# Kernel tuning notes

Hardware: AMD Instinct MI355X
Metric: run time of the kernel (lower is better)

## Reference

```python
import jax, jax.numpy as jnp
import numpy as np

B, N, R = 8, 1024, 8192
D_IN, REL_D = 32, 1
NF_P, NF_R, NF_E, D_OUT = 128, 128, 128, 3
PSTEP = 3


def setup_inputs() -> dict:
    key = jax.random.key(0)
    ks = jax.random.split(key, 26)
    state = jax.random.normal(ks[0], (B, N, D_IN), dtype=jnp.float32)
    # Rr/Rs are one-hot selection matrices [B, N, R]: column j selects the
    # receiver/sender particle of relation j.
    recv = jax.random.randint(ks[1], (B, R), 0, N)
    send = jax.random.randint(ks[2], (B, R), 0, N)
    Rr = jnp.transpose(jax.nn.one_hot(recv, N, dtype=jnp.float32), (0, 2, 1))
    Rs = jnp.transpose(jax.nn.one_hot(send, N, dtype=jnp.float32), (0, 2, 1))
    Ra = jax.random.normal(ks[3], (B, R, REL_D), dtype=jnp.float32)

    def lin(k, i, o):
        kw, kb = jax.random.split(k)
        return (0.02 * jax.random.normal(kw, (i, o), dtype=jnp.float32),
                0.02 * jax.random.normal(kb, (o,), dtype=jnp.float32))

    pe_w0, pe_b0 = lin(ks[4], D_IN, NF_P)
    pe_w1, pe_b1 = lin(ks[5], NF_P, NF_E)
    re_w0, re_b0 = lin(ks[6], 2 * D_IN + REL_D, NF_R)
    re_w1, re_b1 = lin(ks[7], NF_R, NF_R)
    re_w2, re_b2 = lin(ks[8], NF_R, NF_R)
    rp_w, rp_b = lin(ks[9], NF_R + 2 * NF_E, NF_E)   # relation_propagator
    pp_w, pp_b = lin(ks[10], 2 * NF_E, NF_E)          # particle_propagator
    pr_w0, pr_b0 = lin(ks[11], NF_E, NF_E)            # particle_predictor
    pr_w1, pr_b1 = lin(ks[12], NF_E, D_OUT)
    return dict(state=state, Rr=Rr, Rs=Rs, Ra=Ra, pstep=PSTEP,
                pe_w0=pe_w0, pe_b0=pe_b0, pe_w1=pe_w1, pe_b1=pe_b1,
                re_w0=re_w0, re_b0=re_b0, re_w1=re_w1, re_b1=re_b1,
                re_w2=re_w2, re_b2=re_b2, rp_w=rp_w, rp_b=rp_b,
                pp_w=pp_w, pp_b=pp_b, pr_w0=pr_w0, pr_b0=pr_b0,
                pr_w1=pr_w1, pr_b1=pr_b1)


def reference(state, Rr, Rs, Ra, pstep,
              pe_w0, pe_b0, pe_w1, pe_b1,
              re_w0, re_b0, re_w1, re_b1, re_w2, re_b2,
              rp_w, rp_b, pp_w, pp_b,
              pr_w0, pr_b0, pr_w1, pr_b1):
    relu = jax.nn.relu
    # gather particle states into relation slots: Rr^T @ state -> [B, R, D]
    state_r = jnp.einsum('bnr,bnd->brd', Rr, state)
    state_s = jnp.einsum('bnr,bnd->brd', Rs, state)
    # particle encoder: Linear-ReLU-Linear-ReLU
    particle_encode = relu(relu(state @ pe_w0 + pe_b0) @ pe_w1 + pe_b1)  # [B,N,NF_E]
    # relation encoder: 3-layer MLP with ReLU after each layer
    rel_in = jnp.concatenate([state_r, state_s, Ra], axis=2)
    h = relu(rel_in @ re_w0 + re_b0)
    h = relu(h @ re_w1 + re_b1)
    relation_encode = relu(h @ re_w2 + re_b2)  # [B,R,NF_R]

    particle_effect = jnp.zeros((B, N, NF_E), dtype=state.dtype)
    for _ in range(pstep):
        effect_r = jnp.einsum('bnr,bne->bre', Rr, particle_effect)  # gather
        effect_s = jnp.einsum('bnr,bne->bre', Rs, particle_effect)
        rel_x = jnp.concatenate([relation_encode, effect_r, effect_s], axis=2)
        relation_effect = relu(rel_x @ rp_w + rp_b)  # [B,R,NF_E]
        # scatter-add relation effects back to receiver particles
        effect_agg = jnp.einsum('bnr,bre->bne', Rr, relation_effect)
        part_x = jnp.concatenate([particle_encode, effect_agg], axis=2)
        # residual particle propagator: relu(linear(x) + prev_effect)
        particle_effect = relu(part_x @ pp_w + pp_b + particle_effect)
    pred = relu(particle_effect @ pr_w0 + pr_b0) @ pr_w1 + pr_b1  # [B,N,D_OUT]
    return pred
```

## Files before the change

kernel.cpp:

```cpp
#include <hip/hip_runtime.h>

#define NB 8
#define NP 1024
#define NR 8192

typedef unsigned short u16;
typedef __attribute__((ext_vector_type(8))) short bf16x8;
typedef __attribute__((ext_vector_type(4))) float f32x4;
typedef __attribute__((ext_vector_type(4))) unsigned int u32x4;

#define MFMA __builtin_amdgcn_mfma_f32_16x16x32_bf16

static __device__ __forceinline__ float bf2f(u16 u) {
    union { unsigned int i; float f; } v; v.i = ((unsigned int)u) << 16; return v.f;
}
static __device__ __forceinline__ unsigned int f2bf(float f) {
    union { float fv; unsigned int i; } v; v.fv = f;
    unsigned int r = v.i + 0x7FFFu + ((v.i >> 16) & 1u);
    return r >> 16;
}
static __device__ __forceinline__ unsigned int pack2(float a, float b) {
    return f2bf(a) | (f2bf(b) << 16);
}
static __device__ __forceinline__ void unpk8(uint4 v, float* o) {
    o[0] = bf2f((u16)(v.x & 0xFFFF)); o[1] = bf2f((u16)(v.x >> 16));
    o[2] = bf2f((u16)(v.y & 0xFFFF)); o[3] = bf2f((u16)(v.y >> 16));
    o[4] = bf2f((u16)(v.z & 0xFFFF)); o[5] = bf2f((u16)(v.z >> 16));
    o[6] = bf2f((u16)(v.w & 0xFFFF)); o[7] = bf2f((u16)(v.w >> 16));
}

template<int KC>
static __device__ __forceinline__ void load_wfrag(
    const bf16x8* __restrict__ fb, bf16x8 (&wf)[KC][2], int tid)
{
    #pragma unroll
    for (int kc = 0; kc < KC; ++kc)
      #pragma unroll
      for (int nt = 0; nt < 2; ++nt)
        wf[kc][nt] = fb[(kc*2 + nt)*256 + tid];
}

template<int MT, int KC, int LDA>
static __device__ __forceinline__ void mfma_compute(
    const u16* xlds, const bf16x8 (&wf)[KC][2], f32x4 (&acc)[MT][2],
    int l16, int quad)
{
    #pragma unroll
    for (int kc = 0; kc < KC; ++kc) {
        bf16x8 a[MT];
        #pragma unroll
        for (int mt = 0; mt < MT; ++mt)
            a[mt] = *(const bf16x8*)(xlds + (mt*16 + l16)*LDA + kc*32 + quad*8);
        #pragma unroll
        for (int mt = 0; mt < MT; ++mt) {
            acc[mt][0] = MFMA(a[mt], wf[kc][0], acc[mt][0], 0, 0, 0);
            acc[mt][1] = MFMA(a[mt], wf[kc][1], acc[mt][1], 0, 0, 0);
        }
    }
}

template<int MT>
static __device__ __forceinline__ void zero_acc(f32x4 (&acc)[MT][2]) {
    #pragma unroll
    for (int mt = 0; mt < MT; ++mt)
      #pragma unroll
      for (int nt = 0; nt < 2; ++nt)
        acc[mt][nt] = f32x4{0.f, 0.f, 0.f, 0.f};
}

template<int MT, int LDA>
static __device__ __forceinline__ void store_c_lds(
    u16* xlds, const f32x4 (&acc)[MT][2], const float* __restrict__ bias,
    int wave, int quad, int l16, int coloff = 0)
{
    #pragma unroll
    for (int mt = 0; mt < MT; ++mt)
      #pragma unroll
      for (int nt = 0; nt < 2; ++nt) {
        int col = wave*32 + nt*16 + l16;
        float bv = bias[col];
        #pragma unroll
        for (int rg = 0; rg < 4; ++rg)
            xlds[(mt*16 + quad*4 + rg)*LDA + coloff + col] =
                (u16)f2bf(fmaxf(acc[mt][nt][rg] + bv, 0.f));
      }
}

template<int MT, bool RELU>
static __device__ __forceinline__ void store_c_glob(
    u16* __restrict__ out, long row0, const f32x4 (&acc)[MT][2],
    const float* __restrict__ bias, int wave, int quad, int l16)
{
    #pragma unroll
    for (int mt = 0; mt < MT; ++mt)
      #pragma unroll
      for (int nt = 0; nt < 2; ++nt) {
        int col = wave*32 + nt*16 + l16;
        float bv = bias[col];
        #pragma unroll
        for (int rg = 0; rg < 4; ++rg) {
            long r = row0 + mt*16 + quad*4 + rg;
            float v = acc[mt][nt][rg] + bv;
            if (RELU) v = fmaxf(v, 0.f);
            out[r*128 + col] = (u16)f2bf(v);
        }
      }
}

__global__ __launch_bounds__(256) void k_idxprep(
    const u32x4* __restrict__ Rr4, const u32x4* __restrict__ Rs4,
    u16* __restrict__ recv, u16* __restrict__ send,
    const float* __restrict__ w0, const float* __restrict__ w1,
    const float* __restrict__ w2, const float* __restrict__ w3,
    const float* __restrict__ w4, const float* __restrict__ w5,
    const float* __restrict__ w6, const float* __restrict__ w7,
    bf16x8* __restrict__ wfrag,
    const float* __restrict__ state, const float* __restrict__ pe_b0,
    const float* __restrict__ pe_b1, u16* __restrict__ penc)
{
    constexpr int LDA = 136;
    __shared__ __align__(16) u16 xlds[64 * LDA];
    int tid = threadIdx.x;
    const int wave = tid >> 6, quad = (tid >> 4) & 3, l16 = tid & 15;

    if (blockIdx.x < 8) {
        const float* W; int KC, kv, off;
        switch (blockIdx.x) {
            case 0:  W = w0; KC = 3;  kv = 65;  off = 0;  break;
            case 1:  W = w1; KC = 4;  kv = 128; off = 6;  break;
            case 2:  W = w2; KC = 4;  kv = 128; off = 14; break;
            case 3:  W = w3; KC = 1;  kv = 32;  off = 22; break;
            case 4:  W = w4; KC = 4;  kv = 128; off = 24; break;
            case 5:  W = w5; KC = 12; kv = 384; off = 32; break;
            case 6:  W = w6; KC = 8;  kv = 256; off = 56; break;
            default: W = w7; KC = 4;  kv = 128; off = 72; break;
        }
        for (int kc = 0; kc < KC; ++kc)
          for (int nt = 0; nt < 2; ++nt) {
            bf16x8 f;
            #pragma unroll
            for (int j = 0; j < 8; ++j) {
                int k = kc*32 + quad*8 + j;
                f[j] = (k < kv) ? (short)f2bf(W[k*128 + wave*32 + nt*16 + l16]) : (short)0;
            }
            wfrag[(off + kc*2 + nt)*256 + tid] = f;
          }
        return;
    }

    if (blockIdx.x < 136) {
        const long row0 = (long)(blockIdx.x - 8) * 64;
        for (int idx = tid; idx < 64 * 8; idx += 256) {
            int r = idx >> 3, c = idx & 7;
            float4 v = *(const float4*)(state + (row0 + r)*32 + c*4);
            uint2 o; o.x = pack2(v.x, v.y); o.y = pack2(v.z, v.w);
            *(uint2*)(xlds + r*LDA + c*4) = o;
        }
        __syncthreads();
        f32x4 acc[4][2];
        zero_acc<4>(acc);
        {
            bf16x8 wf[1][2];
            #pragma unroll
            for (int nt = 0; nt < 2; ++nt)
              #pragma unroll
              for (int j = 0; j < 8; ++j) {
                int k = quad*8 + j;
                wf[0][nt][j] = (short)f2bf(w3[k*128 + wave*32 + nt*16 + l16]);
              }
            mfma_compute<4, 1, LDA>(xlds, wf, acc, l16, quad);
        }
        __syncthreads();
        store_c_lds<4, LDA>(xlds, acc, pe_b0, wave, quad, l16);
        __syncthreads();
        zero_acc<4>(acc);
        {
            bf16x8 wf[4][2];
            #pragma unroll
            for (int kc = 0; kc < 4; ++kc)
              #pragma unroll
              for (int nt = 0; nt < 2; ++nt)
                #pragma unroll
                for (int j = 0; j < 8; ++j) {
                    int k = kc*32 + quad*8 + j;
                    wf[kc][nt][j] = (short)f2bf(w4[k*128 + wave*32 + nt*16 + l16]);
                }
            mfma_compute<4, 4, LDA>(xlds, wf, acc, l16, quad);
        }
        store_c_glob<4, true>(penc, row0, acc, pe_b1, wave, quad, l16);
        return;
    }

    int sid = blockIdx.x - 136;
    int mat = sid & 1;
    const u32x4* src = mat ? Rs4 : Rr4;
    u16* dst = mat ? send : recv;
    long base = (long)(sid >> 1) * 2048 + tid;
    u32x4 v[8];
    #pragma unroll
    for (int k = 0; k < 8; ++k)
        v[k] = __builtin_nontemporal_load(src + base + k*256);
    #pragma unroll
    for (int k = 0; k < 8; ++k) {
        long i = base + k*256;
        int c4 = (int)(i & 2047), n = (int)((i >> 11) & 1023), b = (int)(i >> 21);
        int o = b * NR + c4 * 4;
        if (v[k][0]) dst[o + 0] = (u16)n;
        if (v[k][1]) dst[o + 1] = (u16)n;
        if (v[k][2]) dst[o + 2] = (u16)n;
        if (v[k][3]) dst[o + 3] = (u16)n;
    }
}

__global__ __launch_bounds__(256) void k_csrenc(
    const float* __restrict__ state, const float* __restrict__ Ra,
    const u16* __restrict__ recv, const u16* __restrict__ send,
    int* __restrict__ row_ptr, unsigned int* __restrict__ pidx,
    const bf16x8* __restrict__ f_re0, const float* __restrict__ re_b0,
    const bf16x8* __restrict__ f_re1, const float* __restrict__ re_b1,
    const bf16x8* __restrict__ f_re2, const float* __restrict__ re_b2,
    const bf16x8* __restrict__ f_rpP, const float* __restrict__ rp_b,
    u16* __restrict__ bufP)
{
    constexpr int LDA = 136;
    __shared__ __align__(16) u16 xlds[64 * LDA];
    __shared__ int cur[NP];
    __shared__ int wsum[4];
    const int tid = threadIdx.x;

    if (blockIdx.x < 8) {
        const int b = blockIdx.x;
        for (int i = tid; i < NP; i += 256) cur[i] = 0;
        __syncthreads();
        int pv[32];
        #pragma unroll
        for (int k = 0; k < 32; ++k) {
            pv[k] = recv[b * NR + k * 256 + tid] & 1023;
            atomicAdd(&cur[pv[k]], 1);
        }
        __syncthreads();
        int4 c4v = ((const int4*)cur)[tid];
        int s = c4v.x + c4v.y + c4v.z + c4v.w;
        int si = s;
        #pragma unroll
        for (int off = 1; off < 64; off <<= 1) {
            int u = __shfl_up(si, off);
            if ((tid & 63) >= off) si += u;
        }
        if ((tid & 63) == 63) wsum[tid >> 6] = si;
        __syncthreads();
        if (tid == 0) {
            int a0 = 0;
            #pragma unroll
            for (int i = 0; i < 4; ++i) { int w = wsum[i]; wsum[i] = a0; a0 += w; }
        }
        __syncthreads();
        int base = si - s + wsum[tid >> 6];
        int e0 = base, e1 = base + c4v.x, e2 = e1 + c4v.y, e3 = e2 + c4v.z;
        int* rp = row_ptr + b * (NP + 1);
        rp[tid*4 + 0] = e0; rp[tid*4 + 1] = e1;
        rp[tid*4 + 2] = e2; rp[tid*4 + 3] = e3;
        cur[tid*4 + 0] = e0; cur[tid*4 + 1] = e1;
        cur[tid*4 + 2] = e2; cur[tid*4 + 3] = e3;
        if (tid == 255) rp[NP] = e3 + c4v.w;
        __syncthreads();
        #pragma unroll
        for (int k = 0; k < 32; ++k) {
            int r = k * 256 + tid;
            int j = atomicAdd(&cur[pv[k]], 1) & 8191;
            pidx[b * NR + j] = (unsigned int)(r & 8191)
                             | ((unsigned int)(send[b * NR + r] & 1023) << 16);
        }
        return;
    }

    const int wave = tid >> 6, quad = (tid >> 4) & 3, l16 = tid & 15;
    f32x4 acc[4][2];
    const int row0 = (blockIdx.x - 8) * 64;
    const int b = row0 >> 13;
    {
        int r = tid >> 2, tt = tid & 3;
        int rel = row0 + r;
        u16* dst = xlds + r * LDA;
        int ri = recv[rel] & 1023;
        int si = send[rel] & 1023;
        const float* rrow = state + ((long)(b*NP + ri)) * 32;
        const float* srow = state + ((long)(b*NP + si)) * 32;
        float4 a0 = *(const float4*)(rrow + tt*8);
        float4 a1 = *(const float4*)(rrow + tt*8 + 4);
        uint4 o;
        o.x = pack2(a0.x, a0.y); o.y = pack2(a0.z, a0.w);
        o.z = pack2(a1.x, a1.y); o.w = pack2(a1.z, a1.w);
        *(uint4*)(dst + tt*8) = o;
        float4 s0 = *(const float4*)(srow + tt*8);
        float4 s1 = *(const float4*)(srow + tt*8 + 4);
        o.x = pack2(s0.x, s0.y); o.y = pack2(s0.z, s0.w);
        o.z = pack2(s1.x, s1.y); o.w = pack2(s1.z, s1.w);
        *(uint4*)(dst + 32 + tt*8) = o;
        if (tt == 3) {
            uint4 z = make_uint4(0, 0, 0, 0);
            *(uint4*)(dst + 64) = z; *(uint4*)(dst + 72) = z;
            *(uint4*)(dst + 80) = z; *(uint4*)(dst + 88) = z;
            dst[64] = (u16)f2bf(Ra[rel]);
        }
    }
    __syncthreads();
    zero_acc<4>(acc);
    {
        bf16x8 wf[3][2];
        load_wfrag<3>(f_re0, wf, tid);
        mfma_compute<4, 3, LDA>(xlds, wf, acc, l16, quad);
    }
    __syncthreads();
    store_c_lds<4, LDA>(xlds, acc, re_b0, wave, quad, l16);
    __syncthreads();
    zero_acc<4>(acc);
    {
        bf16x8 wf[4][2];
        load_wfrag<4>(f_re1, wf, tid);
        mfma_compute<4, 4, LDA>(xlds, wf, acc, l16, quad);
    }
    __syncthreads();
    store_c_lds<4, LDA>(xlds, acc, re_b1, wave, quad, l16);
    __syncthreads();
    zero_acc<4>(acc);
    {
        bf16x8 wf[4][2];
        load_wfrag<4>(f_re2, wf, tid);
        mfma_compute<4, 4, LDA>(xlds, wf, acc, l16, quad);
    }
    __syncthreads();
    store_c_lds<4, LDA>(xlds, acc, re_b2, wave, quad, l16);
    __syncthreads();
    zero_acc<4>(acc);
    {
        bf16x8 wf[4][2];
        load_wfrag<4>(f_rpP, wf, tid);
        mfma_compute<4, 4, LDA>(xlds, wf, acc, l16, quad);
    }
    #pragma unroll
    for (int mt = 0; mt < 4; ++mt)
      #pragma unroll
      for (int nt = 0; nt < 2; ++nt) {
        int col = wave*32 + nt*16 + l16;
        float bv = rp_b[col];
        #pragma unroll
        for (int rg = 0; rg < 4; ++rg) {
            int rl = mt*16 + quad*4 + rg;
            bufP[((long)(row0 + rl))*128 + col] = (u16)f2bf(acc[mt][nt][rg] + bv);
        }
      }
}

template<bool STEP1, bool MAKEUV, bool LAST>
__global__ __launch_bounds__(256) void k_pp(
    const u16* __restrict__ penc, const u16* __restrict__ bufP,
    const u16* __restrict__ UV_in, u16* __restrict__ UV_out,
    const int* __restrict__ row_ptr, const unsigned int* __restrict__ pidx,
    const bf16x8* __restrict__ f_pp, const float* __restrict__ pp_b,
    const bf16x8* __restrict__ f_U, const bf16x8* __restrict__ f_V,
    const bf16x8* __restrict__ f_pr0, const float* __restrict__ pr_b0,
    const float* __restrict__ pr_w1, const float* __restrict__ pr_b1,
    float* __restrict__ peff32_io, float* __restrict__ out)
{
    constexpr int LDA = 264;
    __shared__ __align__(16) u16 xlds[16 * LDA];
    const int tid = threadIdx.x;
    const int wave = tid >> 6, quad = (tid >> 4) & 3, l16 = tid & 15;
    const long row0 = (long)blockIdx.x * 16;

    {
        int r = tid >> 4, c = tid & 15;
        *(uint4*)(xlds + r*LDA + c*8) = *(const uint4*)(penc + (row0 + r)*128 + c*8);
    }
    {
        int pp = tid >> 4;
        int cq = tid & 15;
        int gp = (int)row0 + pp;
        int b = gp >> 10, pl = gp & 1023;
        const int* rp = row_ptr + b * (NP + 1);
        int s0 = rp[pl], e0 = rp[pl + 1];
        const unsigned int* pidxb = pidx + b * NR;
        const u16* bufPb = bufP + (long)b * NR * 128;
        float a[8];
        #pragma unroll
        for (int t = 0; t < 8; ++t) a[t] = 0.f;
        float uv[8];
        if (!STEP1) {
            const u16* ur = UV_in + ((long)gp)*256 + cq*8;
            unpk8(*(const uint4*)ur, uv);
        }
        const u16* uvb = UV_in + ((long)(b*NP))*256 + 128 + cq*8;
        for (int jb = s0; jb < e0; jb += 4) {
            int m = e0 - jb; if (m > 4) m = 4;
            unsigned int ids[4];
            #pragma unroll
            for (int t = 0; t < 4; ++t) {
                int j = jb + t; if (j > e0 - 1) j = e0 - 1;
                ids[t] = pidxb[j];
            }
            uint4 P0[4], V0[4];
            #pragma unroll
            for (int t = 0; t < 4; ++t) {
                P0[t] = *(const uint4*)(bufPb + ((long)(ids[t] & 8191u))*128 + cq*8);
                if (!STEP1)
                    V0[t] = *(const uint4*)(uvb + (long)((ids[t] >> 16) & 1023u)*256);
            }
            #pragma unroll
            for (int t = 0; t < 4; ++t) {
                if (t < m) {
                    float pv[8];
                    unpk8(P0[t], pv);
                    if (STEP1) {
                        #pragma unroll
                        for (int e = 0; e < 8; ++e) a[e] += fmaxf(pv[e], 0.f);
                    } else {
                        float vv[8];
                        unpk8(V0[t], vv);
                        #pragma unroll
                        for (int e = 0; e < 8; ++e)
                            a[e] += fmaxf(pv[e] + uv[e] + vv[e], 0.f);
                    }
                }
            }
        }
        u16* dst = xlds + pp*LDA + 128 + cq*8;
        uint4 o;
        o.x = pack2(a[0], a[1]); o.y = pack2(a[2], a[3]);
        o.z = pack2(a[4], a[5]); o.w = pack2(a[6], a[7]);
        *(uint4*)dst = o;
    }
    __syncthreads();

    f32x4 acc[1][2];
    {
        bf16x8 wf[8][2];
        load_wfrag<8>(f_pp, wf, tid);
        zero_acc<1>(acc);
        mfma_compute<1, 8, LDA>(xlds, wf, acc, l16, quad);
    }
    __syncthreads();

    #pragma unroll
    for (int nt = 0; nt < 2; ++nt) {
        int col = wave*32 + nt*16 + l16;
        float bv = pp_b[col];
        #pragma unroll
        for (int rg = 0; rg < 4; ++rg) {
            int rloc = quad*4 + rg;
            long r = row0 + rloc;
            float prev = STEP1 ? 0.f : peff32_io[r*128 + col];
            float v = fmaxf(acc[0][nt][rg] + bv + prev, 0.f);
            if (!LAST) peff32_io[r*128 + col] = v;
            xlds[rloc*LDA + col] = (u16)f2bf(v);
        }
    }
    __syncthreads();

    if (MAKEUV) {
        #pragma unroll
        for (int half = 0; half < 2; ++half) {
            bf16x8 wf[4][2];
            load_wfrag<4>(half ? f_V : f_U, wf, tid);
            zero_acc<1>(acc);
            mfma_compute<1, 4, LDA>(xlds, wf, acc, l16, quad);
            #pragma unroll
            for (int nt = 0; nt < 2; ++nt) {
                int col = half*128 + wave*32 + nt*16 + l16;
                #pragma unroll
                for (int rg = 0; rg < 4; ++rg) {
                    long r = row0 + quad*4 + rg;
                    UV_out[r*256 + col] = (u16)f2bf(acc[0][nt][rg]);
                }
            }
        }
    }
    if (LAST) {
        bf16x8 wf[4][2];
        load_wfrag<4>(f_pr0, wf, tid);
        zero_acc<1>(acc);
        mfma_compute<1, 4, LDA>(xlds, wf, acc, l16, quad);
        store_c_lds<1, LDA>(xlds, acc, pr_b0, wave, quad, l16, 128);
        __syncthreads();
        if (tid < 48) {
            int row = tid / 3, col = tid - row * 3;
            float s = pr_b1[col];
            const u16* hr = xlds + row * LDA + 128;
            #pragma unroll 8
            for (int k = 0; k < 128; ++k) s += bf2f(hr[k]) * pr_w1[k*3 + col];
            out[(row0 + row)*3 + col] = s;
        }
    }
}

extern "C" void kernel_launch(void* const* d_in, const int* in_sizes, int n_in,
                              void* d_out, int out_size, void* d_ws, size_t ws_size,
                              hipStream_t stream) {
    const float* state = (const float*)d_in[0];
    const float* Rr    = (const float*)d_in[1];
    const float* Rs    = (const float*)d_in[2];
    const float* Ra    = (const float*)d_in[3];
    const float* pe_w0 = (const float*)d_in[5];
    const float* pe_b0 = (const float*)d_in[6];
    const float* pe_w1 = (const float*)d_in[7];
    const float* pe_b1 = (const float*)d_in[8];
    const float* re_w0 = (const float*)d_in[9];
    const float* re_b0 = (const float*)d_in[10];
    const float* re_w1 = (const float*)d_in[11];
    const float* re_b1 = (const float*)d_in[12];
    const float* re_w2 = (const float*)d_in[13];
    const float* re_b2 = (const float*)d_in[14];
    const float* rp_w  = (const float*)d_in[15];
    const float* rp_b  = (const float*)d_in[16];
    const float* pp_w  = (const float*)d_in[17];
    const float* pp_b  = (const float*)d_in[18];
    const float* pr_w0 = (const float*)d_in[19];
    const float* pr_b0 = (const float*)d_in[20];
    const float* pr_w1 = (const float*)d_in[21];
    const float* pr_b1 = (const float*)d_in[22];

    char* p = (char*)d_ws;
    u16*    bufP    = (u16*)p;    p += (size_t)NB*NR*128*2;
    u16*    UVa     = (u16*)p;    p += (size_t)NB*NP*256*2;
    u16*    UVb     = (u16*)p;    p += (size_t)NB*NP*256*2;
    float*  peff32  = (float*)p;  p += (size_t)NB*NP*128*4;
    u16*    penc    = (u16*)p;    p += (size_t)NB*NP*128*2;
    bf16x8* wfrag   = (bf16x8*)p; p += (size_t)80*256*16;
    int*    row_ptr = (int*)p;    p += (size_t)NB*(NP+1)*4 + 12;
    u16*    recv    = (u16*)p;    p += (size_t)NB*NR*2;
    u16*    send    = (u16*)p;    p += (size_t)NB*NR*2;
    unsigned int* pidx = (unsigned int*)p; p += (size_t)NB*NR*4;

    const bf16x8* f_re0 = wfrag + 0*256;
    const bf16x8* f_re1 = wfrag + 6*256;
    const bf16x8* f_re2 = wfrag + 14*256;
    const bf16x8* f_rpP = wfrag + 32*256;
    const bf16x8* f_rpU = wfrag + 40*256;
    const bf16x8* f_rpV = wfrag + 48*256;
    const bf16x8* f_pp  = wfrag + 56*256;
    const bf16x8* f_pr0 = wfrag + 72*256;

    float* outp = (float*)d_out;

    k_idxprep<<<16520, 256, 0, stream>>>((const u32x4*)Rr, (const u32x4*)Rs, recv, send,
                                         re_w0, re_w1, re_w2, pe_w0, pe_w1, rp_w, pp_w, pr_w0,
                                         wfrag, state, pe_b0, pe_b1, penc);
    k_csrenc<<<1032, 256, 0, stream>>>(state, Ra, recv, send, row_ptr, pidx,
                                       f_re0, re_b0, f_re1, re_b1, f_re2, re_b2,
                                       f_rpP, rp_b, bufP);
    k_pp<true,  true,  false><<<512, 256, 0, stream>>>(
        penc, bufP, UVa, UVa, row_ptr, pidx, f_pp, pp_b,
        f_rpU, f_rpV, f_pr0, pr_b0, pr_w1, pr_b1, peff32, outp);
    k_pp<false, true,  false><<<512, 256, 0, stream>>>(
        penc, bufP, UVa, UVb, row_ptr, pidx, f_pp, pp_b,
        f_rpU, f_rpV, f_pr0, pr_b0, pr_w1, pr_b1, peff32, outp);
    k_pp<false, false, true><<<512, 256, 0, stream>>>(
        penc, bufP, UVb, UVa, row_ptr, pidx, f_pp, pp_b,
        f_rpU, f_rpV, f_pr0, pr_b0, pr_w1, pr_b1, peff32, outp);
}
```

Measured before the change: 602.7 us.

## Fuse three propagation steps into one persistent kernel with grid barriers

```diff
diff --git a/kernel.cpp b/kernel.cpp
--- a/kernel.cpp
+++ b/kernel.cpp
@@ -27,6 +27,18 @@
     o[2] = bf2f((u16)(v.y & 0xFFFF)); o[3] = bf2f((u16)(v.y >> 16));
     o[4] = bf2f((u16)(v.z & 0xFFFF)); o[5] = bf2f((u16)(v.z >> 16));
     o[6] = bf2f((u16)(v.w & 0xFFFF)); o[7] = bf2f((u16)(v.w >> 16));
+}
+
+static __device__ __forceinline__ void gbar(int* cnt, int tid, int target) {
+    __syncthreads();
+    if (tid == 0) {
+        __threadfence();
+        atomicAdd(cnt, 1);
+        while (__hip_atomic_load(cnt, __ATOMIC_RELAXED, __HIP_MEMORY_SCOPE_AGENT) < target)
+            __builtin_amdgcn_s_sleep(8);
+        __threadfence();
+    }
+    __syncthreads();
 }
 
 template<int KC>
@@ -195,20 +207,32 @@
     int mat = sid & 1;
     const u32x4* src = mat ? Rs4 : Rr4;
     u16* dst = mat ? send : recv;
-    long base = (long)(sid >> 1) * 2048 + tid;
-    u32x4 v[8];
-    #pragma unroll
-    for (int k = 0; k < 8; ++k)
+    int S = sid >> 1;
+    int r0 = 2*S, r1 = 2*S + 1;
+    u16 n0 = (u16)(r0 & 1023), n1 = (u16)(r1 & 1023);
+    int b0 = r0 >> 10, b1 = r1 >> 10;
+    long base = (long)S * 4096 + tid;
+    u32x4 v[16];
+    #pragma unroll
+    for (int k = 0; k < 16; ++k)
         v[k] = __builtin_nontemporal_load(src + base + k*256);
+    u16* d0 = dst + b0 * NR + tid * 4;
+    u16* d1 = dst + b1 * NR + tid * 4;
     #pragma unroll
     for (int k = 0; k < 8; ++k) {
-        long i = base + k*256;
-        int c4 = (int)(i & 2047), n = (int)((i >> 11) & 1023), b = (int)(i >> 21);
-        int o = b * NR + c4 * 4;
-        if (v[k][0]) dst[o + 0] = (u16)n;
-        if (v[k][1]) dst[o + 1] = (u16)n;
-        if (v[k][2]) dst[o + 2] = (u16)n;
-        if (v[k][3]) dst[o + 3] = (u16)n;
+        int o = k * 1024;
+        if (v[k][0]) d0[o + 0] = n0;
+        if (v[k][1]) d0[o + 1] = n0;
+        if (v[k][2]) d0[o + 2] = n0;
+        if (v[k][3]) d0[o + 3] = n0;
+    }
+    #pragma unroll
+    for (int k = 8; k < 16; ++k) {
+        int o = (k - 8) * 1024;
+        if (v[k][0]) d1[o + 0] = n1;
+        if (v[k][1]) d1[o + 1] = n1;
+        if (v[k][2]) d1[o + 2] = n1;
+        if (v[k][3]) d1[o + 3] = n1;
     }
 }
 
@@ -353,7 +377,8 @@
 }
 
 template<bool STEP1, bool MAKEUV, bool LAST>
-__global__ __launch_bounds__(256) void k_pp(
+static __device__ void pp_body(
+    u16* xlds, int tid, int bid,
     const u16* __restrict__ penc, const u16* __restrict__ bufP,
     const u16* __restrict__ UV_in, u16* __restrict__ UV_out,
     const int* __restrict__ row_ptr, const unsigned int* __restrict__ pidx,
@@ -364,10 +389,8 @@
     float* __restrict__ peff32_io, float* __restrict__ out)
 {
     constexpr int LDA = 264;
-    __shared__ __align__(16) u16 xlds[16 * LDA];
-    const int tid = threadIdx.x;
     const int wave = tid >> 6, quad = (tid >> 4) & 3, l16 = tid & 15;
-    const long row0 = (long)blockIdx.x * 16;
+    const long row0 = (long)bid * 16;
 
     {
         int r = tid >> 4, c = tid & 15;
@@ -491,6 +514,34 @@
             out[(row0 + row)*3 + col] = s;
         }
     }
+}
+
+__global__ __launch_bounds__(256, 2) void k_pp3(
+    const u16* __restrict__ penc, const u16* __restrict__ bufP,
+    u16* __restrict__ UVa, u16* __restrict__ UVb,
+    const int* __restrict__ row_ptr, const unsigned int* __restrict__ pidx,
+    const bf16x8* __restrict__ f_pp, const float* __restrict__ pp_b,
+    const bf16x8* __restrict__ f_U, const bf16x8* __restrict__ f_V,
+    const bf16x8* __restrict__ f_pr0, const float* __restrict__ pr_b0,
+    const float* __restrict__ pr_w1, const float* __restrict__ pr_b1,
+    float* __restrict__ peff32_io, float* __restrict__ out,
+    int* __restrict__ bar)
+{
+    __shared__ __align__(16) u16 xlds[16 * 264];
+    const int tid = threadIdx.x;
+    const int bid = blockIdx.x;
+
+    pp_body<true,  true,  false>(xlds, tid, bid, penc, bufP, UVa, UVa,
+        row_ptr, pidx, f_pp, pp_b, f_U, f_V, f_pr0, pr_b0, pr_w1, pr_b1,
+        peff32_io, out);
+    gbar(bar + 0, tid, 512);
+    pp_body<false, true,  false>(xlds, tid, bid, penc, bufP, UVa, UVb,
+        row_ptr, pidx, f_pp, pp_b, f_U, f_V, f_pr0, pr_b0, pr_w1, pr_b1,
+        peff32_io, out);
+    gbar(bar + 1, tid, 512);
+    pp_body<false, false, true >(xlds, tid, bid, penc, bufP, UVb, UVa,
+        row_ptr, pidx, f_pp, pp_b, f_U, f_V, f_pr0, pr_b0, pr_w1, pr_b1,
+        peff32_io, out);
 }
 
 extern "C" void kernel_launch(void* const* d_in, const int* in_sizes, int n_in,
@@ -530,6 +581,7 @@
     u16*    recv    = (u16*)p;    p += (size_t)NB*NR*2;
     u16*    send    = (u16*)p;    p += (size_t)NB*NR*2;
     unsigned int* pidx = (unsigned int*)p; p += (size_t)NB*NR*4;
+    int*    bar     = (int*)p;    p += 64;
 
     const bf16x8* f_re0 = wfrag + 0*256;
     const bf16x8* f_re1 = wfrag + 6*256;
@@ -542,19 +594,14 @@
 
     float* outp = (float*)d_out;
 
-    k_idxprep<<<16520, 256, 0, stream>>>((const u32x4*)Rr, (const u32x4*)Rs, recv, send,
-                                         re_w0, re_w1, re_w2, pe_w0, pe_w1, rp_w, pp_w, pr_w0,
-                                         wfrag, state, pe_b0, pe_b1, penc);
+    k_idxprep<<<8328, 256, 0, stream>>>((const u32x4*)Rr, (const u32x4*)Rs, recv, send,
+                                        re_w0, re_w1, re_w2, pe_w0, pe_w1, rp_w, pp_w, pr_w0,
+                                        wfrag, state, pe_b0, pe_b1, penc);
     k_csrenc<<<1032, 256, 0, stream>>>(state, Ra, recv, send, row_ptr, pidx,
                                        f_re0, re_b0, f_re1, re_b1, f_re2, re_b2,
                                        f_rpP, rp_b, bufP);
-    k_pp<true,  true,  false><<<512, 256, 0, stream>>>(
-        penc, bufP, UVa, UVa, row_ptr, pidx, f_pp, pp_b,
-        f_rpU, f_rpV, f_pr0, pr_b0, pr_w1, pr_b1, peff32, outp);
-    k_pp<false, true,  false><<<512, 256, 0, stream>>>(
-        penc, bufP, UVa, UVb, row_ptr, pidx, f_pp, pp_b,
-        f_rpU, f_rpV, f_pr0, pr_b0, pr_w1, pr_b1, peff32, outp);
-    k_pp<false, false, true><<<512, 256, 0, stream>>>(
-        penc, bufP, UVb, UVa, row_ptr, pidx, f_pp, pp_b,
-        f_rpU, f_rpV, f_pr0, pr_b0, pr_w1, pr_b1, peff32, outp);
-}
+    hipMemsetAsync(bar, 0, 64, stream);
+    k_pp3<<<512, 256, 0, stream>>>(penc, bufP, UVa, UVb, row_ptr, pidx,
+                                   f_pp, pp_b, f_rpU, f_rpV, f_pr0, pr_b0,
+                                   pr_w1, pr_b1, peff32, outp, bar);
+}
```

Result: slower. 734.1 us (+21.8%).
